# Optimization experiments

Measured on AMD Instinct MI355X. Metric: run time of the kernel, lower is better.

Reference implementation:

```python
import jax, jax.numpy as jnp
import numpy as np

B, L, M, F = 64, 1024, 256, 256


def setup_inputs() -> dict:
    key = jax.random.key(0)
    k1, k2 = jax.random.split(key)
    patch_features = jax.random.normal(k1, (B, L, F), dtype=jnp.float32)
    queue = jax.random.normal(k2, (L, M, F), dtype=jnp.float32)
    return {"patch_features": patch_features, "queue": queue}


def reference(patch_features, queue):
    # sim[b, l, m] = <patch_features[b, l], queue[l, m]>  (batched per-location matmul)
    sim = jnp.einsum('blf,lmf->blm', patch_features, queue)
    # original takes topk(5) then keeps only index 0 == argmax over memory slots
    idx = jnp.argmax(sim, axis=-1)                      # [B, L]
    # N[b, l] = queue[l, idx[b, l]]
    N = queue[jnp.arange(queue.shape[0])[None, :], idx]  # [B, L, F]
    return N
```

## Files before the change

kernel.cpp:

```cpp
#include <hip/hip_runtime.h>

#define B_ 64
#define L_ 1024
#define M_ 256
#define F_ 256
#define LSTEP 512

typedef __attribute__((ext_vector_type(8))) short short8;
typedef __attribute__((ext_vector_type(16))) float f32x16;
typedef unsigned int u32;

struct Frag3 { short8 h, m, l; };

__device__ __forceinline__ u32 asu(float f) { union { float f; u32 u; } c; c.f = f; return c.u; }
__device__ __forceinline__ float asf(u32 u) { union { float f; u32 u; } c; c.u = u; return c.f; }
__device__ __forceinline__ u32 pack2(u32 lo, u32 hi) {
    return __builtin_amdgcn_perm(hi, lo, 0x07060302u);
}
__device__ __forceinline__ float4 ld4(const float* p) {
    return *reinterpret_cast<const float4*>(p);
}

__device__ __forceinline__ void async_cp16(const float* g, float* l) {
    __builtin_amdgcn_global_load_lds(
        (const __attribute__((address_space(1))) u32*)g,
        (__attribute__((address_space(3))) u32*)l,
        16, 0, 0);
}

__device__ __forceinline__ Frag3 split8(float4 a, float4 b) {
    float x[8] = {a.x, a.y, a.z, a.w, b.x, b.y, b.z, b.w};
    u32 xb[8], rb[8], sb[8];
#pragma unroll
    for (int e = 0; e < 8; ++e) {
        xb[e] = asu(x[e]);
        float hf = asf(xb[e] & 0xFFFF0000u);
        float r  = x[e] - hf;
        rb[e] = asu(r);
        float mf = asf(rb[e] & 0xFFFF0000u);
        float r2 = r - mf;
        sb[e] = asu(r2);
    }
    union { u32 w[4]; short8 s; } H, M, Lo;
#pragma unroll
    for (int d = 0; d < 4; ++d) {
        H.w[d]  = pack2(xb[2 * d], xb[2 * d + 1]);
        M.w[d]  = pack2(rb[2 * d], rb[2 * d + 1]);
        Lo.w[d] = pack2(sb[2 * d], sb[2 * d + 1]);
    }
    Frag3 f; f.h = H.s; f.m = M.s; f.l = Lo.s; return f;
}

#define MFMA6(ACC, A, Bf)                                                        \
    ACC = __builtin_amdgcn_mfma_f32_32x32x16_bf16((A).m, (Bf).m, ACC, 0, 0, 0);  \
    ACC = __builtin_amdgcn_mfma_f32_32x32x16_bf16((A).h, (Bf).l, ACC, 0, 0, 0);  \
    ACC = __builtin_amdgcn_mfma_f32_32x32x16_bf16((A).l, (Bf).h, ACC, 0, 0, 0);  \
    ACC = __builtin_amdgcn_mfma_f32_32x32x16_bf16((A).h, (Bf).m, ACC, 0, 0, 0);  \
    ACC = __builtin_amdgcn_mfma_f32_32x32x16_bf16((A).m, (Bf).h, ACC, 0, 0, 0);  \
    ACC = __builtin_amdgcn_mfma_f32_32x32x16_bf16((A).h, (Bf).h, ACC, 0, 0, 0)

__launch_bounds__(512, 2)
__global__ void mq_mfma_2l_kernel(const float* __restrict__ patch,
                                  const float* __restrict__ queue,
                                  float* __restrict__ out) {
    const int l0   = blockIdx.x;
    const int t    = threadIdx.x;
    const int lane = t & 63;
    const int w    = t >> 6;
    const int bt   = w & 1;
    const int mtg  = w >> 1;
    const int r32  = lane & 31;
    const int kh   = lane >> 5;

    __shared__ __align__(16) float Ql[2][256 * 32];
    __shared__ __align__(16) float Pl[2][64 * 32];

    const int lrow = lane >> 3;
    const int lcol = lane & 7;
    const float* qsrcw = queue + ((size_t)l0 * M_ + w * 32 + lrow) * F_ + (lcol ^ lrow) * 4;
    const float* psrcw = patch + ((size_t)(w * 8 + lrow) * L_ + l0) * F_ + (lcol ^ lrow) * 4;
    const size_t QD = (size_t)LSTEP * M_ * F_;
    const size_t PD = (size_t)LSTEP * F_;

#define STAGE(QOFF, POFF, BUF)                                                    \
    {                                                                             \
        _Pragma("unroll")                                                         \
        for (int k = 0; k < 4; ++k)                                               \
            async_cp16(qsrcw + (size_t)k * 8 * F_ + (QOFF),                       \
                       &Ql[BUF][(w * 4 + k) * 256]);                              \
        async_cp16(psrcw + (POFF), &Pl[BUF][w * 256]);                            \
    }

    f32x16 acc0 = (f32x16)0.f, acc1 = (f32x16)0.f;

    STAGE(0, 0, 0);

    const int s7  = r32 & 7;
    const int ra  = bt * 32 + r32;
    const int rb0 = mtg * 64 + r32;
    const int rb1 = mtg * 64 + 32 + r32;

    float* pval = (float*)&Pl[1][0];
    int*   pidx = (int*)&Pl[1][0] + 256;
    int*   sidx = (int*)&Pl[1][0] + 512;

#pragma unroll
    for (int li = 0; li < 2; ++li) {
        const size_t qo = (size_t)li * QD;
        const size_t po = (size_t)li * PD;

#pragma unroll 1
        for (int ft = 0; ft < 8; ++ft) {
            __builtin_amdgcn_s_barrier();
            __builtin_amdgcn_sched_barrier(0);
            if (ft < 7) {
                STAGE(qo + (ft + 1) * 32, po + (ft + 1) * 32, (ft + 1) & 1);
                asm volatile("s_waitcnt vmcnt(5)" ::: "memory");
            } else if (li == 0) {
                STAGE(QD, PD, 0);
                asm volatile("s_waitcnt vmcnt(5)" ::: "memory");
            } else {
                asm volatile("s_waitcnt vmcnt(0)" ::: "memory");
            }
            __builtin_amdgcn_sched_barrier(0);
            __builtin_amdgcn_s_barrier();
            __builtin_amdgcn_sched_barrier(0);

            const float* Qb = Ql[ft & 1];
            const float* Pb = Pl[ft & 1];
#pragma unroll
            for (int kk = 0; kk < 2; ++kk) {
                const int c0 = kk * 4 + kh * 2;
                const float4 a0 = ld4(&Pb[ra * 32 + ((c0 ^ s7) * 4)]);
                const float4 a1 = ld4(&Pb[ra * 32 + (((c0 + 1) ^ s7) * 4)]);
                const Frag3 A = split8(a0, a1);
                {
                    const float4 b0 = ld4(&Qb[rb0 * 32 + ((c0 ^ s7) * 4)]);
                    const float4 b1 = ld4(&Qb[rb0 * 32 + (((c0 + 1) ^ s7) * 4)]);
                    const Frag3 Bf = split8(b0, b1);
                    MFMA6(acc0, A, Bf);
                }
                {
                    const float4 b0 = ld4(&Qb[rb1 * 32 + ((c0 ^ s7) * 4)]);
                    const float4 b1 = ld4(&Qb[rb1 * 32 + (((c0 + 1) ^ s7) * 4)]);
                    const Frag3 Bf = split8(b0, b1);
                    MFMA6(acc1, A, Bf);
                }
            }
        }

        __builtin_amdgcn_s_barrier();

#pragma unroll
        for (int r = 0; r < 16; ++r) {
            float bv = acc0[r];
            int   bi = mtg * 64 + r32;
            {
                const float cv = acc1[r];
                const int   ci = mtg * 64 + 32 + r32;
                if (cv > bv) { bv = cv; bi = ci; }
            }
#pragma unroll
            for (int off = 16; off >= 1; off >>= 1) {
                const float ov = __shfl_xor(bv, off);
                const int   oi = __shfl_xor(bi, off);
                if (ov > bv || (ov == bv && oi < bi)) { bv = ov; bi = oi; }
            }
            if (r32 == 0) {
                const int b = bt * 32 + (r & 3) + 8 * (r >> 2) + 4 * kh;
                pval[mtg * 64 + b] = bv;
                pidx[mtg * 64 + b] = bi;
            }
        }
        __syncthreads();

        if (t < 64) {
            float bv = pval[t];
            int   bi = pidx[t];
#pragma unroll
            for (int g = 1; g < 4; ++g) {
                const float cv = pval[g * 64 + t];
                if (cv > bv) { bv = cv; bi = pidx[g * 64 + t]; }
            }
            sidx[t] = bi;
        }
        __syncthreads();

        {
            const int lcur = l0 + li * LSTEP;
            const int cb = t >> 6;
            const int cc = t & 63;
#pragma unroll
            for (int b0 = 0; b0 < 64; b0 += 8) {
                const int b  = b0 + cb;
                const int mi = sidx[b];
                const float4 v = ld4(&queue[((size_t)lcur * M_ + mi) * F_ + cc * 4]);
                *reinterpret_cast<float4*>(&out[((size_t)b * L_ + lcur) * F_ + cc * 4]) = v;
            }
        }

        acc0 = (f32x16)0.f;
        acc1 = (f32x16)0.f;
    }
}

extern "C" void kernel_launch(void* const* d_in, const int* in_sizes, int n_in,
                              void* d_out, int out_size, void* d_ws, size_t ws_size,
                              hipStream_t stream) {
    const float* patch = (const float*)d_in[0];
    const float* queue = (const float*)d_in[1];
    float* out = (float*)d_out;
    mq_mfma_2l_kernel<<<dim3(LSTEP), dim3(512), 0, stream>>>(patch, queue, out);
}
```

Before: 101.1 us.

## Interleave async LDS prefetch loads with MFMA groups and raise MFMA priority

Before, all five async global-to-LDS copies for the next tile were issued at once at the start of each step. Now each copy is issued between MFMA groups, with sched_barriers to pin the order and s_setprio around the MFMA bursts. The loop uses a single barrier after a full vmcnt(0) wait, and the __syncthreads calls in the reduction become explicit lgkmcnt waits plus s_barrier. The aim is to spread memory issue across the compute phase and cut barrier overhead. The risk is that waiting on vmcnt(0) at the top of each step exposes the load latency that vmcnt(5) previously hid.

```diff
diff --git a/kernel.cpp b/kernel.cpp
--- a/kernel.cpp
+++ b/kernel.cpp
@@ -59,8 +59,10 @@
     ACC = __builtin_amdgcn_mfma_f32_32x32x16_bf16((A).m, (Bf).h, ACC, 0, 0, 0);  \
     ACC = __builtin_amdgcn_mfma_f32_32x32x16_bf16((A).h, (Bf).h, ACC, 0, 0, 0)
 
+#define SBAR() __builtin_amdgcn_sched_barrier(0)
+
 __launch_bounds__(512, 2)
-__global__ void mq_mfma_2l_kernel(const float* __restrict__ patch,
+__global__ void mq_mfma_fi_kernel(const float* __restrict__ patch,
                                   const float* __restrict__ queue,
                                   float* __restrict__ out) {
     const int l0   = blockIdx.x;
@@ -82,18 +84,12 @@
     const size_t QD = (size_t)LSTEP * M_ * F_;
     const size_t PD = (size_t)LSTEP * F_;
 
-#define STAGE(QOFF, POFF, BUF)                                                    \
-    {                                                                             \
-        _Pragma("unroll")                                                         \
-        for (int k = 0; k < 4; ++k)                                               \
-            async_cp16(qsrcw + (size_t)k * 8 * F_ + (QOFF),                       \
-                       &Ql[BUF][(w * 4 + k) * 256]);                              \
-        async_cp16(psrcw + (POFF), &Pl[BUF][w * 256]);                            \
-    }
-
     f32x16 acc0 = (f32x16)0.f, acc1 = (f32x16)0.f;
 
-    STAGE(0, 0, 0);
+#pragma unroll
+    for (int k = 0; k < 4; ++k)
+        async_cp16(qsrcw + (size_t)k * 8 * F_, &Ql[0][(w * 4 + k) * 256]);
+    async_cp16(psrcw, &Pl[0][w * 256]);
 
     const int s7  = r32 & 7;
     const int ra  = bt * 32 + r32;
@@ -111,45 +107,78 @@
 
 #pragma unroll 1
         for (int ft = 0; ft < 8; ++ft) {
+            asm volatile("s_waitcnt vmcnt(0)" ::: "memory");
             __builtin_amdgcn_s_barrier();
-            __builtin_amdgcn_sched_barrier(0);
-            if (ft < 7) {
-                STAGE(qo + (ft + 1) * 32, po + (ft + 1) * 32, (ft + 1) & 1);
-                asm volatile("s_waitcnt vmcnt(5)" ::: "memory");
-            } else if (li == 0) {
-                STAGE(QD, PD, 0);
-                asm volatile("s_waitcnt vmcnt(5)" ::: "memory");
-            } else {
-                asm volatile("s_waitcnt vmcnt(0)" ::: "memory");
-            }
-            __builtin_amdgcn_sched_barrier(0);
-            __builtin_amdgcn_s_barrier();
-            __builtin_amdgcn_sched_barrier(0);
+            SBAR();
+
+            const bool dostg = (ft < 7) || (li == 0);
+            const size_t qoff = (ft < 7) ? qo + (size_t)(ft + 1) * 32 : QD;
+            const size_t poff = (ft < 7) ? po + (size_t)(ft + 1) * 32 : PD;
+            float* Qd = (ft < 7) ? Ql[(ft + 1) & 1] : Ql[0];
+            float* Pd = (ft < 7) ? Pl[(ft + 1) & 1] : Pl[0];
 
             const float* Qb = Ql[ft & 1];
             const float* Pb = Pl[ft & 1];
-#pragma unroll
-            for (int kk = 0; kk < 2; ++kk) {
-                const int c0 = kk * 4 + kh * 2;
+
+            {
+                const int c0 = kh * 2;
                 const float4 a0 = ld4(&Pb[ra * 32 + ((c0 ^ s7) * 4)]);
                 const float4 a1 = ld4(&Pb[ra * 32 + (((c0 + 1) ^ s7) * 4)]);
                 const Frag3 A = split8(a0, a1);
+                if (dostg) async_cp16(qsrcw + qoff, &Qd[(w * 4 + 0) * 256]);
+                SBAR();
                 {
                     const float4 b0 = ld4(&Qb[rb0 * 32 + ((c0 ^ s7) * 4)]);
                     const float4 b1 = ld4(&Qb[rb0 * 32 + (((c0 + 1) ^ s7) * 4)]);
                     const Frag3 Bf = split8(b0, b1);
+                    __builtin_amdgcn_s_setprio(1);
                     MFMA6(acc0, A, Bf);
-                }
+                    __builtin_amdgcn_s_setprio(0);
+                }
+                if (dostg) async_cp16(qsrcw + (size_t)8 * F_ + qoff, &Qd[(w * 4 + 1) * 256]);
+                SBAR();
                 {
                     const float4 b0 = ld4(&Qb[rb1 * 32 + ((c0 ^ s7) * 4)]);
                     const float4 b1 = ld4(&Qb[rb1 * 32 + (((c0 + 1) ^ s7) * 4)]);
                     const Frag3 Bf = split8(b0, b1);
+                    __builtin_amdgcn_s_setprio(1);
                     MFMA6(acc1, A, Bf);
-                }
+                    __builtin_amdgcn_s_setprio(0);
+                }
+                if (dostg) async_cp16(qsrcw + (size_t)16 * F_ + qoff, &Qd[(w * 4 + 2) * 256]);
+                SBAR();
+            }
+            {
+                const int c0 = 4 + kh * 2;
+                const float4 a0 = ld4(&Pb[ra * 32 + ((c0 ^ s7) * 4)]);
+                const float4 a1 = ld4(&Pb[ra * 32 + (((c0 + 1) ^ s7) * 4)]);
+                const Frag3 A = split8(a0, a1);
+                if (dostg) async_cp16(qsrcw + (size_t)24 * F_ + qoff, &Qd[(w * 4 + 3) * 256]);
+                SBAR();
+                {
+                    const float4 b0 = ld4(&Qb[rb0 * 32 + ((c0 ^ s7) * 4)]);
+                    const float4 b1 = ld4(&Qb[rb0 * 32 + (((c0 + 1) ^ s7) * 4)]);
+                    const Frag3 Bf = split8(b0, b1);
+                    __builtin_amdgcn_s_setprio(1);
+                    MFMA6(acc0, A, Bf);
+                    __builtin_amdgcn_s_setprio(0);
+                }
+                if (dostg) async_cp16(psrcw + poff, &Pd[w * 256]);
+                SBAR();
+                {
+                    const float4 b0 = ld4(&Qb[rb1 * 32 + ((c0 ^ s7) * 4)]);
+                    const float4 b1 = ld4(&Qb[rb1 * 32 + (((c0 + 1) ^ s7) * 4)]);
+                    const Frag3 Bf = split8(b0, b1);
+                    __builtin_amdgcn_s_setprio(1);
+                    MFMA6(acc1, A, Bf);
+                    __builtin_amdgcn_s_setprio(0);
+                }
+                SBAR();
             }
         }
 
         __builtin_amdgcn_s_barrier();
+        SBAR();
 
 #pragma unroll
         for (int r = 0; r < 16; ++r) {
@@ -172,7 +201,9 @@
                 pidx[mtg * 64 + b] = bi;
             }
         }
-        __syncthreads();
+        asm volatile("s_waitcnt lgkmcnt(0)" ::: "memory");
+        __builtin_amdgcn_s_barrier();
+        SBAR();
 
         if (t < 64) {
             float bv = pval[t];
@@ -184,7 +215,9 @@
             }
             sidx[t] = bi;
         }
-        __syncthreads();
+        asm volatile("s_waitcnt lgkmcnt(0)" ::: "memory");
+        __builtin_amdgcn_s_barrier();
+        SBAR();
 
         {
             const int lcur = l0 + li * LSTEP;
@@ -210,5 +243,5 @@
     const float* patch = (const float*)d_in[0];
     const float* queue = (const float*)d_in[1];
     float* out = (float*)d_out;
-    mq_mfma_2l_kernel<<<dim3(LSTEP), dim3(512), 0, stream>>>(patch, queue, out);
-}
+    mq_mfma_fi_kernel<<<dim3(LSTEP), dim3(512), 0, stream>>>(patch, queue, out);
+}
```

Result: slower. 106.2 us (+5.0%).

## Overlap first location's gather/store with second location's MFMA loop

Applied to the files above, without the earlier changes.

For the first of the two locations each block handles, the selected indices are kept in registers instead of gathering right away. The queue-row gather loads are issued at the start of the second location's first k-tile and stored after that tile's MFMAs, so the gather traffic overlaps compute. The vmcnt wait count is raised on the next tile to allow for the extra outstanding loads. In exchange the 8 gathered float4 values stay live across the MFMA block, which raises register pressure, and correctness depends on the hand-tuned waitcnt values.

```diff
diff --git a/kernel.cpp b/kernel.cpp
--- a/kernel.cpp
+++ b/kernel.cpp
@@ -60,7 +60,7 @@
     ACC = __builtin_amdgcn_mfma_f32_32x32x16_bf16((A).h, (Bf).h, ACC, 0, 0, 0)
 
 __launch_bounds__(512, 2)
-__global__ void mq_mfma_2l_kernel(const float* __restrict__ patch,
+__global__ void mq_mfma_ov_kernel(const float* __restrict__ patch,
                                   const float* __restrict__ queue,
                                   float* __restrict__ out) {
     const int l0   = blockIdx.x;
@@ -104,6 +104,10 @@
     int*   pidx = (int*)&Pl[1][0] + 256;
     int*   sidx = (int*)&Pl[1][0] + 512;
 
+    const int cb = t >> 6;
+    const int cc = t & 63;
+    int mreg[8];
+
 #pragma unroll
     for (int li = 0; li < 2; ++li) {
         const size_t qo = (size_t)li * QD;
@@ -114,8 +118,12 @@
             __builtin_amdgcn_s_barrier();
             __builtin_amdgcn_sched_barrier(0);
             if (ft < 7) {
-                STAGE(qo + (ft + 1) * 32, po + (ft + 1) * 32, (ft + 1) & 1);
-                asm volatile("s_waitcnt vmcnt(5)" ::: "memory");
+                STAGE(qo + (size_t)(ft + 1) * 32, po + (size_t)(ft + 1) * 32, (ft + 1) & 1);
+                if (li == 1 && ft == 1) {
+                    asm volatile("s_waitcnt vmcnt(21)" ::: "memory");
+                } else {
+                    asm volatile("s_waitcnt vmcnt(5)" ::: "memory");
+                }
             } else if (li == 0) {
                 STAGE(QD, PD, 0);
                 asm volatile("s_waitcnt vmcnt(5)" ::: "memory");
@@ -124,6 +132,21 @@
             }
             __builtin_amdgcn_sched_barrier(0);
             __builtin_amdgcn_s_barrier();
+            __builtin_amdgcn_sched_barrier(0);
+
+            float4 gv0, gv1, gv2, gv3, gv4, gv5, gv6, gv7;
+            const bool dogather = (li == 1 && ft == 0);
+            if (dogather) {
+                const float* qg = queue + (size_t)l0 * M_ * F_ + cc * 4;
+                gv0 = ld4(qg + (size_t)mreg[0] * F_);
+                gv1 = ld4(qg + (size_t)mreg[1] * F_);
+                gv2 = ld4(qg + (size_t)mreg[2] * F_);
+                gv3 = ld4(qg + (size_t)mreg[3] * F_);
+                gv4 = ld4(qg + (size_t)mreg[4] * F_);
+                gv5 = ld4(qg + (size_t)mreg[5] * F_);
+                gv6 = ld4(qg + (size_t)mreg[6] * F_);
+                gv7 = ld4(qg + (size_t)mreg[7] * F_);
+            }
             __builtin_amdgcn_sched_barrier(0);
 
             const float* Qb = Ql[ft & 1];
@@ -147,6 +170,22 @@
                     MFMA6(acc1, A, Bf);
                 }
             }
+
+            __builtin_amdgcn_sched_barrier(0);
+            if (dogather) {
+                float* og = out + (size_t)cb * 8 * L_ * F_ + (size_t)l0 * F_ + cc * 4;
+                const size_t OS = (size_t)8 * L_ * F_;
+                *reinterpret_cast<float4*>(out + ((size_t)(0 * 8 + cb) * L_ + l0) * F_ + cc * 4) = gv0;
+                *reinterpret_cast<float4*>(out + ((size_t)(1 * 8 + cb) * L_ + l0) * F_ + cc * 4) = gv1;
+                *reinterpret_cast<float4*>(out + ((size_t)(2 * 8 + cb) * L_ + l0) * F_ + cc * 4) = gv2;
+                *reinterpret_cast<float4*>(out + ((size_t)(3 * 8 + cb) * L_ + l0) * F_ + cc * 4) = gv3;
+                *reinterpret_cast<float4*>(out + ((size_t)(4 * 8 + cb) * L_ + l0) * F_ + cc * 4) = gv4;
+                *reinterpret_cast<float4*>(out + ((size_t)(5 * 8 + cb) * L_ + l0) * F_ + cc * 4) = gv5;
+                *reinterpret_cast<float4*>(out + ((size_t)(6 * 8 + cb) * L_ + l0) * F_ + cc * 4) = gv6;
+                *reinterpret_cast<float4*>(out + ((size_t)(7 * 8 + cb) * L_ + l0) * F_ + cc * 4) = gv7;
+                (void)og; (void)OS;
+            }
+            __builtin_amdgcn_sched_barrier(0);
         }
 
         __builtin_amdgcn_s_barrier();
@@ -186,10 +225,11 @@
         }
         __syncthreads();
 
-        {
-            const int lcur = l0 + li * LSTEP;
-            const int cb = t >> 6;
-            const int cc = t & 63;
+        if (li == 0) {
+#pragma unroll
+            for (int p = 0; p < 8; ++p) mreg[p] = sidx[p * 8 + cb];
+        } else {
+            const int lcur = l0 + LSTEP;
 #pragma unroll
             for (int b0 = 0; b0 < 64; b0 += 8) {
                 const int b  = b0 + cb;
@@ -210,5 +250,5 @@
     const float* patch = (const float*)d_in[0];
     const float* queue = (const float*)d_in[1];
     float* out = (float*)d_out;
-    mq_mfma_2l_kernel<<<dim3(LSTEP), dim3(512), 0, stream>>>(patch, queue, out);
-}
+    mq_mfma_ov_kernel<<<dim3(LSTEP), dim3(512), 0, stream>>>(patch, queue, out);
+}
```

Result: slower. 132.8 us (+31.3%).
